# Optimization experiments

Measured on AMD Instinct MI355X. Metric: run time of the kernel, lower is better.

Reference implementation:

```python
import jax, jax.numpy as jnp
import numpy as np

B, FH, FW, T = 128, 26, 26, 50
A, NUM_CLASSES = 5, 20
IGNORE_THRESH = 0.75
COORD_SCALE, NOOBJ_SCALE, OBJ_SCALE, CLASS_SCALE = 1.0, 1.0, 5.0, 1.0
ANCHORS = jnp.array([[1.3221, 1.73145], [3.19275, 4.00944], [5.05587, 8.09892],
                     [9.47112, 4.84053], [11.2364, 10.0071]], dtype=jnp.float32)


def xywh2xxyy(b):
    return jnp.stack([b[:, 0] - b[:, 2] / 2, b[:, 1] - b[:, 3] / 2,
                      b[:, 0] + b[:, 2] / 2, b[:, 1] + b[:, 3] / 2], axis=1)


def xxyy2xywh(b):
    return jnp.stack([(b[:, 0] + b[:, 2]) / 2, (b[:, 1] + b[:, 3]) / 2,
                      b[:, 2] - b[:, 0], b[:, 3] - b[:, 1]], axis=1)


def pair_iou(b1, b2):
    # b1: [N,4] xxyy, b2: [K,4] xxyy -> [N,K]
    xi1 = jnp.maximum(b1[:, None, 0], b2[None, :, 0])
    yi1 = jnp.maximum(b1[:, None, 1], b2[None, :, 1])
    xi2 = jnp.minimum(b1[:, None, 2], b2[None, :, 2])
    yi2 = jnp.minimum(b1[:, None, 3], b2[None, :, 3])
    inter = jnp.maximum(xi2 - xi1, 0.0) * jnp.maximum(yi2 - yi1, 0.0)
    a1 = ((b1[:, 2] - b1[:, 0]) * (b1[:, 3] - b1[:, 1]))[:, None]
    a2 = ((b2[:, 2] - b2[:, 0]) * (b2[:, 3] - b2[:, 1]))[None, :]
    return inter / (a1 + a2 - inter)


def make_all_anchors(F_H, F_W):
    ys, xs = jnp.meshgrid(jnp.arange(F_H), jnp.arange(F_W), indexing='ij')
    cells = jnp.stack([xs.ravel(), ys.ravel()], axis=-1).astype(jnp.float32)  # [K,2] (c_x, c_y)
    K = F_H * F_W
    all_anch = jnp.concatenate([jnp.broadcast_to(cells[:, None, :], (K, A, 2)),
                                jnp.broadcast_to(ANCHORS[None, :, :], (K, A, 2))], axis=-1)
    return all_anch.reshape(K * A, 4)  # (c_x, c_y, p_w, p_h), top-left-cell coords


def _build_target_single(box_deltas, gt, all_anch, anch_xxyy, F_H, F_W):
    # box_deltas: [K*A,4] (sig tx, sig ty, exp tw, exp th); gt: [T,5]
    K = F_H * F_W
    valid = gt[:, :4].sum(-1) > 0
    scale = jnp.array([F_W, F_H, F_W, F_H], dtype=jnp.float32)
    gt_xxyy = gt[:, :4] * scale  # [T,4] grid units
    # predicted boxes
    pred = jnp.stack([all_anch[:, 0] + box_deltas[:, 0], all_anch[:, 1] + box_deltas[:, 1],
                      all_anch[:, 2] * box_deltas[:, 2], all_anch[:, 3] * box_deltas[:, 3]], axis=1)
    pred_xxyy = xywh2xxyy(pred)
    ious = pair_iou(pred_xxyy, gt_xxyy)                       # [K*A, T]
    ious = jnp.where(valid[None, :], ious, -1.0)
    max_iou = ious.max(axis=-1)                               # [K*A]
    pos_any = jnp.any(max_iou > IGNORE_THRESH)
    iou_mask0 = jnp.where(pos_any & (max_iou >= IGNORE_THRESH), 0.0, NOOBJ_SCALE).reshape(K, A)
    # anchor-gt overlaps for responsibility assignment
    overlaps = pair_iou(anch_xxyy, gt_xxyy).reshape(K, A, T)
    gt_xcycwh = xxyy2xywh(gt_xxyy)                            # [T,4]
    cx = jnp.clip(jnp.floor(gt_xcycwh[:, 0]).astype(jnp.int32), 0, F_W - 1)
    cy = jnp.clip(jnp.floor(gt_xcycwh[:, 1]).astype(jnp.int32), 0, F_H - 1)
    cell = cy * F_W + cx                                      # [T]
    aidx = jnp.argmax(overlaps[cell, :, jnp.arange(T)], axis=-1)  # [T]
    anch_ka = all_anch.reshape(K, A, 4)
    assigned = anch_ka[cell, aidx]                            # [T,4]
    tgt_box = jnp.stack([gt_xcycwh[:, 0] - assigned[:, 0], gt_xcycwh[:, 1] - assigned[:, 1],
                         gt_xcycwh[:, 2] / assigned[:, 2], gt_xcycwh[:, 3] / assigned[:, 3]], axis=1)
    miou_t = max_iou.reshape(K, A)[cell, aidx]                # [T]
    cls_t = gt[:, 4]
    carry0 = (jnp.zeros((K, A)), iou_mask0, jnp.zeros((K, A, 4)),
              jnp.zeros((K, A)), jnp.zeros((K, A)), jnp.zeros((K, A)))
    def step(c, xs):
        it, im, bt, bm, ct, cm = c
        ce, an, v, tb, cl, mi = xs
        def w(arr, new):
            return arr.at[ce, an].set(jnp.where(v, new, arr[ce, an]))
        return (w(it, mi), w(im, OBJ_SCALE), w(bt, tb), w(bm, 1.0), w(ct, cl), w(cm, 1.0)), None
    (it, im, bt, bm, ct, cm), _ = jax.lax.scan(step, carry0, (cell, aidx, valid, tgt_box, cls_t, miou_t))
    return it, im, bt, bm, ct, cm


def setup_inputs() -> dict:
    key = jax.random.key(0)
    k1, k2, k3, k4, k5 = jax.random.split(key, 5)
    outputs = jax.random.normal(k1, (B, A * (5 + NUM_CLASSES), FH, FW), dtype=jnp.float32) * 0.1
    x1 = jax.random.uniform(k2, (B, T, 1), minval=0.02, maxval=0.75)
    y1 = jax.random.uniform(k3, (B, T, 1), minval=0.02, maxval=0.75)
    wh = jax.random.uniform(k4, (B, T, 2), minval=0.05, maxval=0.2)
    cls = jax.random.randint(k5, (B, T, 1), 0, NUM_CLASSES).astype(jnp.float32)
    targets = jnp.concatenate([x1, y1, x1 + wh[..., :1], y1 + wh[..., 1:]], axis=-1)
    targets = jnp.concatenate([targets, cls], axis=-1)  # [B, T, 5]
    return {"outputs": outputs, "targets": targets}


def reference(outputs, targets):
    Bn, _, F_H, F_W = outputs.shape
    out = outputs.transpose(0, 2, 3, 1).reshape(Bn, F_H * F_W * A, 5 + NUM_CLASSES)
    xy = jax.nn.sigmoid(out[..., 0:2])
    wh = jnp.exp(out[..., 2:4])
    conf = jax.nn.sigmoid(out[..., 4])            # [B, K*A]
    cls_score = out[..., 5:]                      # [B, K*A, C]
    box_delta = jnp.concatenate([xy, wh], axis=-1)  # [B, K*A, 4]
    all_anch = make_all_anchors(F_H, F_W)
    anch_xcycwh = all_anch.at[:, :2].add(0.5)
    anch_xxyy = xywh2xxyy(anch_xcycwh)
    it, im, bt, bm, ct, cm = jax.vmap(
        lambda d, g: _build_target_single(d, g, all_anch, anch_xxyy, F_H, F_W))(box_delta, targets)
    it = it.reshape(Bn, -1)
    im = im.reshape(Bn, -1)
    bt = bt.reshape(Bn, -1, 4)
    bm = bm.reshape(Bn, -1, 1)
    ct = ct.reshape(Bn, -1).astype(jnp.int32)
    cm = cm.reshape(Bn, -1)
    box_loss = COORD_SCALE * jnp.sum((box_delta * bm - bt * bm) ** 2) / 2.0 / Bn
    iou_loss = jnp.sum((conf * im - it * im) ** 2) / 2.0 / Bn
    logp = jax.nn.log_softmax(cls_score, axis=-1)
    ce = -jnp.take_along_axis(logp, ct[..., None], axis=-1)[..., 0]
    class_loss = CLASS_SCALE * jnp.sum(cm * ce) / Bn
    return box_loss + iou_loss + class_loss
```

## Files before the change

### kernel.cpp

```cpp
#include <hip/hip_runtime.h>
#include <math.h>

constexpr int BN = 128;
constexpr int FH = 26, FW = 26;
constexpr int T  = 50;
constexpr int A  = 5;
constexpr int NC = 20;
constexpr int K  = FH * FW;
constexpr int KA = K * A;
constexpr int CH = A * (5 + NC);

constexpr float IGNORE_THRESH = 0.75f;
constexpr float OBJ_SCALE = 5.0f;

constexpr int GCH   = (KA + 255) / 256;
constexpr int NPART = BN * GCH;

__constant__ float ANCW[A] = {1.3221f, 3.19275f, 5.05587f, 9.47112f, 11.2364f};
__constant__ float ANCH[A] = {1.73145f, 4.00944f, 8.09892f, 4.84053f, 10.0071f};

__device__ __forceinline__ float fast_sigmoid(float x) {
    return __builtin_amdgcn_rcpf(1.0f + __expf(-x));
}

__global__ __launch_bounds__(256) void yolo_main(
        const float* __restrict__ outputs,
        const float* __restrict__ targets,
        float* __restrict__ Lp, float* __restrict__ Mp, int* __restrict__ Anyp) {
    __shared__ float4 sbox[T];
    __shared__ float4 stb[T];
    __shared__ float  scls[T];
    __shared__ float  sg3[T];
    __shared__ int    wtab[256];
    __shared__ float  redl[4], redm[4];
    __shared__ int    reda[4];

    const int b    = blockIdx.y;
    const int tid  = threadIdx.x;
    const int base = blockIdx.x * 256;
    const int s    = base + tid;
    const bool live = s < KA;

    const int a = live ? (s / K) : 0;
    const int k = live ? (s - a * K) : 0;
    const float* ob = outputs + (size_t)b * CH * K + (size_t)(a * 25) * K;
    float o0 = 0, o1 = 0, o2 = 0, o3 = 0, o4 = 0;
    if (live) {
        o0 = ob[0 * K + k];
        o1 = ob[1 * K + k];
        o2 = ob[2 * K + k];
        o3 = ob[3 * K + k];
        o4 = ob[4 * K + k];
    }

    wtab[tid] = -1;
    int myslot = -1;
    if (tid < T) {
        const float* gt = targets + ((size_t)b * T + tid) * 5;
        float rx1 = gt[0], ry1 = gt[1], rx2 = gt[2], ry2 = gt[3];
        bool valid = (rx1 + ry1 + rx2 + ry2) > 0.0f;
        float x1 = rx1 * FW, y1 = ry1 * FH, x2 = rx2 * FW, y2 = ry2 * FH;
        float w = x2 - x1, h = y2 - y1;

        float cxf = 0.5f * (x1 + x2), cyf = 0.5f * (y1 + y2);
        int cx = (int)floorf(cxf); cx = min(max(cx, 0), FW - 1);
        int cy = (int)floorf(cyf); cy = min(max(cy, 0), FH - 1);
        int cell = cy * FW + cx;

        float acx = (float)cx + 0.5f, acy = (float)cy + 0.5f;
        float best = -1.0f; int ai = 0;
        for (int aa = 0; aa < A; ++aa) {
            float aw = ANCW[aa], ah = ANCH[aa];
            float xi1 = fmaxf(acx - 0.5f * aw, x1), yi1 = fmaxf(acy - 0.5f * ah, y1);
            float xi2 = fminf(acx + 0.5f * aw, x2), yi2 = fminf(acy + 0.5f * ah, y2);
            float inter = fmaxf(xi2 - xi1, 0.0f) * fmaxf(yi2 - yi1, 0.0f);
            float iou = inter / (aw * ah + w * h - inter);
            if (iou > best) { best = iou; ai = aa; }
        }

        float4 sb = valid ? make_float4(x1, y1, x2, y2)
                          : make_float4(1e18f, 1e18f, -1e18f, -1e18f);
        sbox[tid] = sb;
        sg3[tid]  = 3.0f * ((sb.z - sb.x) * (sb.w - sb.y));
        stb[tid]  = make_float4(cxf - (float)cx, cyf - (float)cy,
                                w / ANCW[ai], h / ANCH[ai]);
        scls[tid] = gt[4];
        if (valid) myslot = ai * K + cell;
    }
    __syncthreads();

    if (myslot >= 0) {
        int local = myslot - base;
        if ((unsigned)local < 256u) atomicMax(&wtab[local], tid);
    }
    __syncthreads();

    float loss = 0.0f, masked = 0.0f;
    int anyf = 0;

    if (live) {
        const int yy = k / FW, xx = k - yy * FW;
        float s0 = fast_sigmoid(o0), s1 = fast_sigmoid(o1);
        float e2 = __expf(o2),       e3 = __expf(o3);
        float px = (float)xx + s0, py = (float)yy + s1;
        float pw = ANCW[a] * e2,  ph = ANCH[a] * e3;
        float px1 = px - 0.5f * pw, px2 = px + 0.5f * pw;
        float py1 = py - 0.5f * ph, py2 = py + 0.5f * ph;
        float parea = pw * ph;
        float pa3   = 3.0f * parea;

        const int w = wtab[tid];
        const bool heavy = __any(w >= 0);

        float m = -1.0f;
        bool p_ge, p_gt;
        if (heavy) {
            #pragma unroll 10
            for (int t = 0; t < T; ++t) {
                float4 bx = sbox[t];
                float garea = (bx.z - bx.x) * (bx.w - bx.y);
                float xi1 = fmaxf(px1, bx.x), yi1 = fmaxf(py1, bx.y);
                float xi2 = fminf(px2, bx.z), yi2 = fminf(py2, bx.w);
                float iw = fmaxf(xi2 - xi1, 0.0f), ih = fmaxf(yi2 - yi1, 0.0f);
                float inter = iw * ih;
                float iou = inter * __builtin_amdgcn_rcpf(parea + garea - inter);
                m = fmaxf(m, iou);
            }
            p_gt = (m >  IGNORE_THRESH);
            p_ge = (m >= IGNORE_THRESH);
        } else {
            float dmax = -INFINITY;
            #pragma unroll 10
            for (int t = 0; t < T; ++t) {
                float4 bx = sbox[t];
                float xi1 = fmaxf(px1, bx.x), yi1 = fmaxf(py1, bx.y);
                float xi2 = fminf(px2, bx.z), yi2 = fminf(py2, bx.w);
                float iw = fmaxf(xi2 - xi1, 0.0f), ih = fmaxf(yi2 - yi1, 0.0f);
                float i7 = (iw * ih) * 7.0f;
                dmax = fmaxf(dmax, i7 - (pa3 + sg3[t]));
            }
            p_gt = (dmax >  0.0f);
            p_ge = (dmax >= 0.0f);
        }
        anyf = p_gt ? 1 : 0;

        float conf = fast_sigmoid(o4);
        if (w >= 0) {
            float d = (conf - m) * OBJ_SCALE;
            loss += 0.5f * d * d;
            float4 tb = stb[w];
            float d0 = s0 - tb.x, d1 = s1 - tb.y;
            float d2 = e2 - tb.z, d3 = e3 - tb.w;
            loss += 0.5f * (d0 * d0 + d1 * d1 + d2 * d2 + d3 * d3);

            float v[NC];
            float mx = -3.402823466e38f;
            #pragma unroll
            for (int c = 0; c < NC; ++c) {
                v[c] = ob[(5 + c) * K + k];
                mx = fmaxf(mx, v[c]);
            }
            const int cls = (int)scls[w];
            float se = 0.0f, vc = 0.0f;
            #pragma unroll
            for (int c = 0; c < NC; ++c) {
                se += __expf(v[c] - mx);
                vc = (c == cls) ? v[c] : vc;
            }
            loss += (__logf(se) + mx) - vc;
        } else {
            float term = 0.5f * conf * conf;
            loss += term;
            if (p_ge) masked += term;
        }
    }

    for (int off = 32; off > 0; off >>= 1) {
        loss   += __shfl_down(loss, off);
        masked += __shfl_down(masked, off);
    }
    anyf = __any(anyf) ? 1 : 0;
    int lane = tid & 63, wv = tid >> 6;
    if (lane == 0) { redl[wv] = loss; redm[wv] = masked; reda[wv] = anyf; }
    __syncthreads();
    if (tid == 0) {
        int idx = b * GCH + blockIdx.x;
        Lp[idx]   = redl[0] + redl[1] + redl[2] + redl[3];
        Mp[idx]   = redm[0] + redm[1] + redm[2] + redm[3];
        Anyp[idx] = reda[0] | reda[1] | reda[2] | reda[3];
    }
}

__global__ __launch_bounds__(128) void yolo_fix(
        const float* __restrict__ Lp, const float* __restrict__ Mp,
        const int* __restrict__ Anyp, float* __restrict__ out) {
    __shared__ float red[2];
    int tid = threadIdx.x;
    float L = 0.0f, M = 0.0f;
    int any = 0;
    if (tid < BN) {
        #pragma unroll
        for (int c = 0; c < GCH; ++c) {
            int idx = tid * GCH + c;
            L += Lp[idx];
            M += Mp[idx];
            any |= Anyp[idx];
        }
    }
    float acc = L - (any ? M : 0.0f);
    for (int off = 32; off > 0; off >>= 1) acc += __shfl_down(acc, off);
    if ((tid & 63) == 0) red[tid >> 6] = acc;
    __syncthreads();
    if (tid == 0) out[0] = (red[0] + red[1]) * (1.0f / (float)BN);
}

extern "C" void kernel_launch(void* const* d_in, const int* in_sizes, int n_in,
                              void* d_out, int out_size, void* d_ws, size_t ws_size,
                              hipStream_t stream) {
    const float* outputs = (const float*)d_in[0];
    const float* targets = (const float*)d_in[1];
    float* out = (float*)d_out;

    float* Lp   = (float*)d_ws;
    float* Mp   = Lp + NPART;
    int*   Anyp = (int*)(Mp + NPART);

    yolo_main<<<dim3(GCH, BN), 256, 0, stream>>>(outputs, targets, Lp, Mp, Anyp);
    yolo_fix<<<1, 128, 0, stream>>>(Lp, Mp, Anyp, out);
}
```

Baseline: 96.49 us.

## Process two adjacent anchor cells per thread with float2 loads

Each thread now handles two horizontally adjacent cells of the same anchor. It loads the five box channels as float2 vectors and reuses each shared-memory ground-truth box read for both IoU computations. The block covers 512 slots, which halves the grid and changes the wtab indexing. The precomputed ga3 table is dropped and recomputed inside the loop. This raises per-thread register use and lowers the thread count, which may reduce latency hiding.

Result: faster. 93.29 us (-3.3%).

```diff
diff --git a/kernel.cpp b/kernel.cpp
--- a/kernel.cpp
+++ b/kernel.cpp
@@ -9,11 +9,13 @@
 constexpr int K  = FH * FW;
 constexpr int KA = K * A;
 constexpr int CH = A * (5 + NC);
+constexpr int KP = K / 2;
+constexpr int PAIRS = KA / 2;
 
 constexpr float IGNORE_THRESH = 0.75f;
 constexpr float OBJ_SCALE = 5.0f;
 
-constexpr int GCH   = (KA + 255) / 256;
+constexpr int GCH   = (PAIRS + 255) / 256;
 constexpr int NPART = BN * GCH;
 
 __constant__ float ANCW[A] = {1.3221f, 3.19275f, 5.05587f, 9.47112f, 11.2364f};
@@ -30,30 +32,32 @@
     __shared__ float4 sbox[T];
     __shared__ float4 stb[T];
     __shared__ float  scls[T];
-    __shared__ float  sg3[T];
-    __shared__ int    wtab[256];
+    __shared__ int    wtab[512];
     __shared__ float  redl[4], redm[4];
     __shared__ int    reda[4];
 
-    const int b    = blockIdx.y;
-    const int tid  = threadIdx.x;
-    const int base = blockIdx.x * 256;
-    const int s    = base + tid;
-    const bool live = s < KA;
-
-    const int a = live ? (s / K) : 0;
-    const int k = live ? (s - a * K) : 0;
+    const int b   = blockIdx.y;
+    const int tid = threadIdx.x;
+    const int p   = blockIdx.x * 256 + tid;
+    const bool live = p < PAIRS;
+
+    const int a  = live ? (p / KP) : 0;
+    const int kk = live ? (p - a * KP) : 0;
+    const int k0 = kk * 2;
+
     const float* ob = outputs + (size_t)b * CH * K + (size_t)(a * 25) * K;
-    float o0 = 0, o1 = 0, o2 = 0, o3 = 0, o4 = 0;
+    float2 o0 = {0.f, 0.f}, o1 = {0.f, 0.f}, o2 = {0.f, 0.f},
+           o3 = {0.f, 0.f}, o4 = {0.f, 0.f};
     if (live) {
-        o0 = ob[0 * K + k];
-        o1 = ob[1 * K + k];
-        o2 = ob[2 * K + k];
-        o3 = ob[3 * K + k];
-        o4 = ob[4 * K + k];
-    }
-
-    wtab[tid] = -1;
+        o0 = *(const float2*)(ob + 0 * K + k0);
+        o1 = *(const float2*)(ob + 1 * K + k0);
+        o2 = *(const float2*)(ob + 2 * K + k0);
+        o3 = *(const float2*)(ob + 3 * K + k0);
+        o4 = *(const float2*)(ob + 4 * K + k0);
+    }
+
+    wtab[tid]       = -1;
+    wtab[tid + 256] = -1;
     int myslot = -1;
     if (tid < T) {
         const float* gt = targets + ((size_t)b * T + tid) * 5;
@@ -78,10 +82,8 @@
             if (iou > best) { best = iou; ai = aa; }
         }
 
-        float4 sb = valid ? make_float4(x1, y1, x2, y2)
+        sbox[tid] = valid ? make_float4(x1, y1, x2, y2)
                           : make_float4(1e18f, 1e18f, -1e18f, -1e18f);
-        sbox[tid] = sb;
-        sg3[tid]  = 3.0f * ((sb.z - sb.x) * (sb.w - sb.y));
         stb[tid]  = make_float4(cxf - (float)cx, cyf - (float)cy,
                                 w / ANCW[ai], h / ANCH[ai]);
         scls[tid] = gt[4];
@@ -90,8 +92,8 @@
     __syncthreads();
 
     if (myslot >= 0) {
-        int local = myslot - base;
-        if ((unsigned)local < 256u) atomicMax(&wtab[local], tid);
+        int local = myslot - blockIdx.x * 512;
+        if ((unsigned)local < 512u) atomicMax(&wtab[local], tid);
     }
     __syncthreads();
 
@@ -99,68 +101,87 @@
     int anyf = 0;
 
     if (live) {
-        const int yy = k / FW, xx = k - yy * FW;
-        float s0 = fast_sigmoid(o0), s1 = fast_sigmoid(o1);
-        float e2 = __expf(o2),       e3 = __expf(o3);
-        float px = (float)xx + s0, py = (float)yy + s1;
-        float pw = ANCW[a] * e2,  ph = ANCH[a] * e3;
-        float px1 = px - 0.5f * pw, px2 = px + 0.5f * pw;
-        float py1 = py - 0.5f * ph, py2 = py + 0.5f * ph;
-        float parea = pw * ph;
-        float pa3   = 3.0f * parea;
-
-        const int w = wtab[tid];
-        const bool heavy = __any(w >= 0);
-
-        float m = -1.0f;
-        bool p_ge, p_gt;
+        const int yy = k0 / FW, xx = k0 - yy * FW;
+        const float aw = ANCW[a], ah = ANCH[a];
+
+        float sA0 = fast_sigmoid(o0.x), sA1 = fast_sigmoid(o1.x);
+        float eA2 = __expf(o2.x),       eA3 = __expf(o3.x);
+        float sB0 = fast_sigmoid(o0.y), sB1 = fast_sigmoid(o1.y);
+        float eB2 = __expf(o2.y),       eB3 = __expf(o3.y);
+
+        float pxA = (float)xx + sA0,       pyA = (float)yy + sA1;
+        float pwA = aw * eA2,              phA = ah * eA3;
+        float pxB = (float)(xx + 1) + sB0, pyB = (float)yy + sB1;
+        float pwB = aw * eB2,              phB = ah * eB3;
+
+        float ax1 = pxA - 0.5f * pwA, ax2 = pxA + 0.5f * pwA;
+        float ay1 = pyA - 0.5f * phA, ay2 = pyA + 0.5f * phA;
+        float bx1_ = pxB - 0.5f * pwB, bx2_ = pxB + 0.5f * pwB;
+        float by1_ = pyB - 0.5f * phB, by2_ = pyB + 0.5f * phB;
+        float areaA = pwA * phA, areaB = pwB * phB;
+        float pa3A = 3.0f * areaA, pa3B = 3.0f * areaB;
+
+        const int w0 = wtab[2 * tid], w1 = wtab[2 * tid + 1];
+        const bool heavy = __any((w0 >= 0) || (w1 >= 0));
+
+        float mA = -1.0f, mB = -1.0f;
+        bool geA, gtA, geB, gtB;
         if (heavy) {
             #pragma unroll 10
             for (int t = 0; t < T; ++t) {
                 float4 bx = sbox[t];
                 float garea = (bx.z - bx.x) * (bx.w - bx.y);
-                float xi1 = fmaxf(px1, bx.x), yi1 = fmaxf(py1, bx.y);
-                float xi2 = fminf(px2, bx.z), yi2 = fminf(py2, bx.w);
+                float xi1 = fmaxf(ax1, bx.x), yi1 = fmaxf(ay1, bx.y);
+                float xi2 = fminf(ax2, bx.z), yi2 = fminf(ay2, bx.w);
                 float iw = fmaxf(xi2 - xi1, 0.0f), ih = fmaxf(yi2 - yi1, 0.0f);
                 float inter = iw * ih;
-                float iou = inter * __builtin_amdgcn_rcpf(parea + garea - inter);
-                m = fmaxf(m, iou);
-            }
-            p_gt = (m >  IGNORE_THRESH);
-            p_ge = (m >= IGNORE_THRESH);
+                mA = fmaxf(mA, inter * __builtin_amdgcn_rcpf(areaA + garea - inter));
+                xi1 = fmaxf(bx1_, bx.x); yi1 = fmaxf(by1_, bx.y);
+                xi2 = fminf(bx2_, bx.z); yi2 = fminf(by2_, bx.w);
+                iw = fmaxf(xi2 - xi1, 0.0f); ih = fmaxf(yi2 - yi1, 0.0f);
+                inter = iw * ih;
+                mB = fmaxf(mB, inter * __builtin_amdgcn_rcpf(areaB + garea - inter));
+            }
+            gtA = (mA >  IGNORE_THRESH); geA = (mA >= IGNORE_THRESH);
+            gtB = (mB >  IGNORE_THRESH); geB = (mB >= IGNORE_THRESH);
         } else {
-            float dmax = -INFINITY;
+            float dA = -INFINITY, dB = -INFINITY;
             #pragma unroll 10
             for (int t = 0; t < T; ++t) {
                 float4 bx = sbox[t];
-                float xi1 = fmaxf(px1, bx.x), yi1 = fmaxf(py1, bx.y);
-                float xi2 = fminf(px2, bx.z), yi2 = fminf(py2, bx.w);
+                float ga3 = 3.0f * ((bx.z - bx.x) * (bx.w - bx.y));
+                float xi1 = fmaxf(ax1, bx.x), yi1 = fmaxf(ay1, bx.y);
+                float xi2 = fminf(ax2, bx.z), yi2 = fminf(ay2, bx.w);
                 float iw = fmaxf(xi2 - xi1, 0.0f), ih = fmaxf(yi2 - yi1, 0.0f);
-                float i7 = (iw * ih) * 7.0f;
-                dmax = fmaxf(dmax, i7 - (pa3 + sg3[t]));
-            }
-            p_gt = (dmax >  0.0f);
-            p_ge = (dmax >= 0.0f);
-        }
-        anyf = p_gt ? 1 : 0;
-
-        float conf = fast_sigmoid(o4);
-        if (w >= 0) {
-            float d = (conf - m) * OBJ_SCALE;
+                dA = fmaxf(dA, (iw * ih) * 7.0f - (pa3A + ga3));
+                xi1 = fmaxf(bx1_, bx.x); yi1 = fmaxf(by1_, bx.y);
+                xi2 = fminf(bx2_, bx.z); yi2 = fminf(by2_, bx.w);
+                iw = fmaxf(xi2 - xi1, 0.0f); ih = fmaxf(yi2 - yi1, 0.0f);
+                dB = fmaxf(dB, (iw * ih) * 7.0f - (pa3B + ga3));
+            }
+            gtA = (dA >  0.0f); geA = (dA >= 0.0f);
+            gtB = (dB >  0.0f); geB = (dB >= 0.0f);
+        }
+        anyf = (gtA || gtB) ? 1 : 0;
+
+        float confA = fast_sigmoid(o4.x), confB = fast_sigmoid(o4.y);
+
+        if (w0 >= 0) {
+            float d = (confA - mA) * OBJ_SCALE;
             loss += 0.5f * d * d;
-            float4 tb = stb[w];
-            float d0 = s0 - tb.x, d1 = s1 - tb.y;
-            float d2 = e2 - tb.z, d3 = e3 - tb.w;
+            float4 tb = stb[w0];
+            float d0 = sA0 - tb.x, d1 = sA1 - tb.y;
+            float d2 = eA2 - tb.z, d3 = eA3 - tb.w;
             loss += 0.5f * (d0 * d0 + d1 * d1 + d2 * d2 + d3 * d3);
 
             float v[NC];
             float mx = -3.402823466e38f;
             #pragma unroll
             for (int c = 0; c < NC; ++c) {
-                v[c] = ob[(5 + c) * K + k];
+                v[c] = ob[(5 + c) * K + k0];
                 mx = fmaxf(mx, v[c]);
             }
-            const int cls = (int)scls[w];
+            const int cls = (int)scls[w0];
             float se = 0.0f, vc = 0.0f;
             #pragma unroll
             for (int c = 0; c < NC; ++c) {
@@ -169,9 +190,38 @@
             }
             loss += (__logf(se) + mx) - vc;
         } else {
-            float term = 0.5f * conf * conf;
+            float term = 0.5f * confA * confA;
             loss += term;
-            if (p_ge) masked += term;
+            if (geA) masked += term;
+        }
+
+        if (w1 >= 0) {
+            float d = (confB - mB) * OBJ_SCALE;
+            loss += 0.5f * d * d;
+            float4 tb = stb[w1];
+            float d0 = sB0 - tb.x, d1 = sB1 - tb.y;
+            float d2 = eB2 - tb.z, d3 = eB3 - tb.w;
+            loss += 0.5f * (d0 * d0 + d1 * d1 + d2 * d2 + d3 * d3);
+
+            float v[NC];
+            float mx = -3.402823466e38f;
+            #pragma unroll
+            for (int c = 0; c < NC; ++c) {
+                v[c] = ob[(5 + c) * K + k0 + 1];
+                mx = fmaxf(mx, v[c]);
+            }
+            const int cls = (int)scls[w1];
+            float se = 0.0f, vc = 0.0f;
+            #pragma unroll
+            for (int c = 0; c < NC; ++c) {
+                se += __expf(v[c] - mx);
+                vc = (c == cls) ? v[c] : vc;
+            }
+            loss += (__logf(se) + mx) - vc;
+        } else {
+            float term = 0.5f * confB * confB;
+            loss += term;
+            if (geB) masked += term;
         }
     }
 
```
